# Kernel optimization log

Hardware: AMD Instinct MI355X
Metric: run time of the kernel (lower is better)

## Reference

```python
import jax, jax.numpy as jnp
import numpy as np

N = 100000   # num nodes
E = 20000    # num hyperedges
D = 128      # feature dim
NNZ = 600000 # incidences
EPS = 1e-5


def setup_inputs() -> dict:
    key = jax.random.key(0)
    ks = jax.random.split(key, 16)
    src = jax.random.randint(ks[0], (NNZ,), 0, N)   # node indices
    edg = jax.random.randint(ks[1], (NNZ,), 0, E)   # hyperedge indices
    edge_index = jnp.stack([src, edg]).astype(jnp.int64)
    node_attr = jax.random.normal(ks[2], (N, D), jnp.float32)
    edge_attr = jax.random.normal(ks[3], (E, D), jnp.float32)  # unused by forward
    inp = {"edge_index": edge_index, "node_attr": node_attr, "edge_attr": edge_attr}
    for l in range(3):
        inp[f"W{l+1}"] = jax.random.normal(ks[4 + l], (D, D), jnp.float32) / np.float32(np.sqrt(D))
        inp[f"b{l+1}"] = jnp.zeros((D,), jnp.float32)
        inp[f"g{l+1}"] = jnp.ones((D,), jnp.float32)
        inp[f"beta{l+1}"] = jnp.zeros((D,), jnp.float32)
    return inp


def _hconv(x, W, b, src, edg):
    # PyG HypergraphConv (no attention): out = D^{-1} H W_e B^{-1} H^T (X Theta) + b, W_e = I
    x = x @ W
    ones = jnp.ones(src.shape, x.dtype)
    deg_n = jax.ops.segment_sum(ones, src, num_segments=N)  # node degree
    deg_e = jax.ops.segment_sum(ones, edg, num_segments=E)  # hyperedge size
    Dinv = jnp.where(deg_n > 0, 1.0 / deg_n, 0.0)
    Binv = jnp.where(deg_e > 0, 1.0 / deg_e, 0.0)
    # node -> hyperedge: m_e = B^{-1} sum_{i in e} x_i
    e_feat = Binv[:, None] * jax.ops.segment_sum(x[src], edg, num_segments=E)
    # hyperedge -> node: out_i = D^{-1} sum_{e ni i} m_e
    out = Dinv[:, None] * jax.ops.segment_sum(e_feat[edg], src, num_segments=N)
    return out + b


def _bn(x, g, beta):
    # BatchNorm1d, training mode (biased variance over nodes)
    mu = jnp.mean(x, axis=0)
    var = jnp.mean((x - mu) ** 2, axis=0)
    return g * (x - mu) / jnp.sqrt(var + EPS) + beta


def reference(edge_index, node_attr, edge_attr,
              W1, b1, g1, beta1, W2, b2, g2, beta2, W3, b3, g3, beta3):
    src, edg = edge_index[0], edge_index[1]
    x = _bn(jax.nn.relu(_hconv(node_attr, W1, b1, src, edg)), g1, beta1)
    x = _bn(jax.nn.relu(_hconv(x, W2, b2, src, edg)), g2, beta2)
    x = _bn(jax.nn.relu(_hconv(x, W3, b3, src, edg)), g3, beta3)
    return x
```

## Files before the change

### kernel.cpp

```cpp
#include <hip/hip_runtime.h>
#include <stdint.h>

#define DIM 128

static inline int cdiv(long a, long b) { return (int)((a + b - 1) / b); }

typedef float f32x4 __attribute__((ext_vector_type(4)));

__device__ __forceinline__ unsigned pk_bf16(float a, float b) {
  unsigned ua = __float_as_uint(a), ub = __float_as_uint(b);
  ua = (ua + 0x7FFFu + ((ua >> 16) & 1u)) >> 16;
  ub = (ub + 0x7FFFu + ((ub >> 16) & 1u)) >> 16;
  return ua | (ub << 16);
}
__device__ __forceinline__ float bf_lo(unsigned u) { return __uint_as_float(u << 16); }
__device__ __forceinline__ float bf_hi(unsigned u) { return __uint_as_float(u & 0xFFFF0000u); }

__global__ __launch_bounds__(256) void convert_idx_kernel(
    const int* __restrict__ raw, int* __restrict__ out, long n_total) {
  bool is64;
  {
    int l = threadIdx.x & 63;
    int v = raw[2 * l + 1];
    unsigned long long m = __ballot(v == 0);
    is64 = (m == ~0ull);
  }
  long i = blockIdx.x * 256L + threadIdx.x;
  if (i < n_total) out[i] = is64 ? raw[2 * i] : raw[i];
}

__global__ __launch_bounds__(256) void count_kernel(
    const int* __restrict__ src, const int* __restrict__ edg,
    int* __restrict__ cnt, int E, int nnz) {
  int g = blockIdx.x * 256 + threadIdx.x;
  if (g < nnz) {
    atomicAdd(&cnt[edg[g]], 1);
    atomicAdd(&cnt[E + src[g]], 1);
  }
}

__global__ __launch_bounds__(256) void scanA_kernel(
    const int* __restrict__ cnt, int* __restrict__ P, int* __restrict__ BS, int M) {
  __shared__ int lds[256];
  int t = threadIdx.x;
  long base = blockIdx.x * 1024L;
  int v[4], ts = 0;
#pragma unroll
  for (int j = 0; j < 4; ++j) {
    long i = base + t * 4 + j;
    v[j] = (i < M) ? cnt[i] : 0;
    ts += v[j];
  }
  lds[t] = ts;
  __syncthreads();
  for (int off = 1; off < 256; off <<= 1) {
    int x = (t >= off) ? lds[t - off] : 0;
    __syncthreads();
    lds[t] += x;
    __syncthreads();
  }
  int run = lds[t] - ts;
#pragma unroll
  for (int j = 0; j < 4; ++j) {
    long i = base + t * 4 + j;
    if (i < M) P[i] = run;
    run += v[j];
  }
  if (t == 255) BS[blockIdx.x] = lds[255];
}

__global__ void scanB_kernel(int* __restrict__ BS, int* __restrict__ P,
                             int nblocks, int M) {
  if (threadIdx.x == 0) {
    int run = 0;
    for (int i = 0; i < nblocks; ++i) { int x = BS[i]; BS[i] = run; run += x; }
    P[M] = run;
  }
}

__global__ __launch_bounds__(256) void scanC_kernel(
    int* __restrict__ P, const int* __restrict__ BS, int M) {
  long i = blockIdx.x * 256L + threadIdx.x;
  if (i < M) P[i] += BS[i >> 10];
}

__global__ __launch_bounds__(256) void fill_adj_kernel(
    const int* __restrict__ src, const int* __restrict__ edg,
    const int* __restrict__ P, int* __restrict__ cnt,
    int* __restrict__ adj_e, int* __restrict__ adj_n, int E, int nnz) {
  int g = blockIdx.x * 256 + threadIdx.x;
  if (g < nnz) {
    int e = edg[g], s = src[g];
    int pe = P[e] + atomicAdd(&cnt[e], 1);
    adj_e[pe] = s;
    int pn = P[E + s] - nnz + atomicAdd(&cnt[E + s], 1);
    adj_n[pn] = e;
  }
}

__global__ void prep_w_kernel(const float* __restrict__ W,
                              const float* __restrict__ aff_a,
                              const float* __restrict__ aff_d,
                              float* __restrict__ Wp, float* __restrict__ rvec,
                              int has_aff) {
  int j = threadIdx.x;
  float racc = 0.0f;
  for (int c = 0; c < DIM; ++c) {
    float w = W[c * DIM + j];
    float a = has_aff ? aff_a[c] : 1.0f;
    float d = has_aff ? aff_d[c] : 0.0f;
    Wp[c * DIM + j] = a * w;
    racc = fmaf(d, w, racc);
  }
  rvec[j] = racc;
}

__global__ __launch_bounds__(256) void cast_x_kernel(
    const float* __restrict__ X, uint2* __restrict__ xh, long total4) {
  long i = blockIdx.x * 256L + threadIdx.x;
  if (i >= total4) return;
  float4 v = ((const float4*)X)[i];
  uint2 o;
  o.x = pk_bf16(v.x, v.y);
  o.y = pk_bf16(v.z, v.w);
  xh[i] = o;
}

__global__ __launch_bounds__(256) void edge_gather_kernel(
    const uint2* __restrict__ xh, const int* __restrict__ P,
    const int* __restrict__ adj_e, float* __restrict__ ag, int E, int SENT) {
  int slot = threadIdx.x >> 5;
  int l = threadIdx.x & 31;
  int e = blockIdx.x * 8 + slot;
  if (e >= E) return;
  int p0 = P[e], p1 = P[e + 1];
  float4 a = {0.f, 0.f, 0.f, 0.f};
  int kl = p1 - 1;
  for (int k = p0; k < p1; k += 8) {
    int n0 = adj_e[min(k, kl)];
    int n1 = (k + 1 <= kl) ? adj_e[k + 1] : SENT;
    int n2 = (k + 2 <= kl) ? adj_e[k + 2] : SENT;
    int n3 = (k + 3 <= kl) ? adj_e[k + 3] : SENT;
    int n4 = (k + 4 <= kl) ? adj_e[k + 4] : SENT;
    int n5 = (k + 5 <= kl) ? adj_e[k + 5] : SENT;
    int n6 = (k + 6 <= kl) ? adj_e[k + 6] : SENT;
    int n7 = (k + 7 <= kl) ? adj_e[k + 7] : SENT;
    uint2 q0 = xh[(size_t)n0 * 32 + l];
    uint2 q1 = xh[(size_t)n1 * 32 + l];
    uint2 q2 = xh[(size_t)n2 * 32 + l];
    uint2 q3 = xh[(size_t)n3 * 32 + l];
    uint2 q4 = xh[(size_t)n4 * 32 + l];
    uint2 q5 = xh[(size_t)n5 * 32 + l];
    uint2 q6 = xh[(size_t)n6 * 32 + l];
    uint2 q7 = xh[(size_t)n7 * 32 + l];
    a.x += ((bf_lo(q0.x) + bf_lo(q1.x)) + (bf_lo(q2.x) + bf_lo(q3.x))) +
           ((bf_lo(q4.x) + bf_lo(q5.x)) + (bf_lo(q6.x) + bf_lo(q7.x)));
    a.y += ((bf_hi(q0.x) + bf_hi(q1.x)) + (bf_hi(q2.x) + bf_hi(q3.x))) +
           ((bf_hi(q4.x) + bf_hi(q5.x)) + (bf_hi(q6.x) + bf_hi(q7.x)));
    a.z += ((bf_lo(q0.y) + bf_lo(q1.y)) + (bf_lo(q2.y) + bf_lo(q3.y))) +
           ((bf_lo(q4.y) + bf_lo(q5.y)) + (bf_lo(q6.y) + bf_lo(q7.y)));
    a.w += ((bf_hi(q0.y) + bf_hi(q1.y)) + (bf_hi(q2.y) + bf_hi(q3.y))) +
           ((bf_hi(q4.y) + bf_hi(q5.y)) + (bf_hi(q6.y) + bf_hi(q7.y)));
  }
  float binv = (p1 > p0) ? 1.0f / (float)(p1 - p0) : 0.0f;
  float4 o;
  o.x = a.x * binv; o.y = a.y * binv; o.z = a.z * binv; o.w = a.w * binv;
  ((float4*)ag)[(size_t)e * 32 + l] = o;
}

__global__ __launch_bounds__(256) void gemm128_kernel(
    const float* __restrict__ X, const float* __restrict__ Wp,
    const float* __restrict__ rvec, const int* __restrict__ Pdeg,
    unsigned* __restrict__ Yh, int nrows) {
  __shared__ float sW[32 * DIM];
  __shared__ float sX[DIM * 36];
  const int t = threadIdx.x;
  const int row0 = blockIdx.x * DIM;
  const int tx = t & 15, ty = t >> 4;
  const int col0 = tx * 8, lr0 = ty * 8;
  float acc[8][8];
#pragma unroll
  for (int i = 0; i < 8; ++i)
#pragma unroll
    for (int j = 0; j < 8; ++j) acc[i][j] = 0.0f;

  for (int kc = 0; kc < 4; ++kc) {
    __syncthreads();
    {
      const float4* W4 = (const float4*)(Wp + kc * 32 * DIM);
      float4* sW4 = (float4*)sW;
#pragma unroll
      for (int i = 0; i < 4; ++i) sW4[t + i * 256] = W4[t + i * 256];
    }
#pragma unroll
    for (int i = 0; i < 4; ++i) {
      int q = t + i * 256;
      int rr = q >> 3, kq = q & 7;
      int gr = row0 + rr; if (gr >= nrows) gr = nrows - 1;
      float4 v = *(const float4*)&X[(size_t)gr * DIM + kc * 32 + kq * 4];
      *(float4*)&sX[rr * 36 + kq * 4] = v;
    }
    __syncthreads();
    for (int kk = 0; kk < 32; ++kk) {
      float4 w0 = *(const float4*)&sW[kk * DIM + col0];
      float4 w1 = *(const float4*)&sW[kk * DIM + col0 + 4];
      float wv[8] = {w0.x, w0.y, w0.z, w0.w, w1.x, w1.y, w1.z, w1.w};
      float xv[8];
#pragma unroll
      for (int i = 0; i < 8; ++i) xv[i] = sX[(lr0 + i) * 36 + kk];
#pragma unroll
      for (int i = 0; i < 8; ++i)
#pragma unroll
        for (int j = 0; j < 8; ++j) acc[i][j] = fmaf(xv[i], wv[j], acc[i][j]);
    }
  }
  float4 r0 = *(const float4*)&rvec[col0];
  float4 r1 = *(const float4*)&rvec[col0 + 4];
#pragma unroll
  for (int i = 0; i < 8; ++i) {
    int gr = row0 + lr0 + i;
    if (gr < nrows) {
      float nz = (Pdeg[gr + 1] > Pdeg[gr]) ? 1.0f : 0.0f;
      float o0x = (acc[i][0] + r0.x) * nz, o0y = (acc[i][1] + r0.y) * nz;
      float o0z = (acc[i][2] + r0.z) * nz, o0w = (acc[i][3] + r0.w) * nz;
      float o1x = (acc[i][4] + r1.x) * nz, o1y = (acc[i][5] + r1.y) * nz;
      float o1z = (acc[i][6] + r1.z) * nz, o1w = (acc[i][7] + r1.w) * nz;
      uint4 st;
      st.x = pk_bf16(o0x, o0y);
      st.y = pk_bf16(o0z, o0w);
      st.z = pk_bf16(o1x, o1y);
      st.w = pk_bf16(o1z, o1w);
      *(uint4*)&Yh[(size_t)gr * 64 + (col0 >> 1)] = st;
    }
  }
}

__global__ __launch_bounds__(256) void node_gather_kernel(
    const uint2* __restrict__ ef, const int* __restrict__ P,
    const int* __restrict__ adj_n, const float* __restrict__ b,
    uint2* __restrict__ zh, float* __restrict__ sum,
    float* __restrict__ sumsq, int E, int N, int nnz, int SENT) {
  __shared__ float lsum[DIM], lsumsq[DIM];
  int t = threadIdx.x;
  if (t < DIM) { lsum[t] = 0.f; lsumsq[t] = 0.f; }
  __syncthreads();
  int slot = t >> 5;
  int l = t & 31;
  float4 bc = ((const float4*)b)[l];
  float4 s1 = {0.f, 0.f, 0.f, 0.f}, s2 = {0.f, 0.f, 0.f, 0.f};
  for (int i = blockIdx.x * 8 + slot; i < N; i += gridDim.x * 8) {
    int p0 = P[E + i] - nnz, p1 = P[E + i + 1] - nnz;
    float4 a = {0.f, 0.f, 0.f, 0.f};
    int kl = p1 - 1;
    for (int k = p0; k < p1; k += 8) {
      int e0 = adj_n[min(k, kl)];
      int e1 = (k + 1 <= kl) ? adj_n[k + 1] : SENT;
      int e2 = (k + 2 <= kl) ? adj_n[k + 2] : SENT;
      int e3 = (k + 3 <= kl) ? adj_n[k + 3] : SENT;
      int e4 = (k + 4 <= kl) ? adj_n[k + 4] : SENT;
      int e5 = (k + 5 <= kl) ? adj_n[k + 5] : SENT;
      int e6 = (k + 6 <= kl) ? adj_n[k + 6] : SENT;
      int e7 = (k + 7 <= kl) ? adj_n[k + 7] : SENT;
      uint2 q0 = ef[(size_t)e0 * 32 + l];
      uint2 q1 = ef[(size_t)e1 * 32 + l];
      uint2 q2 = ef[(size_t)e2 * 32 + l];
      uint2 q3 = ef[(size_t)e3 * 32 + l];
      uint2 q4 = ef[(size_t)e4 * 32 + l];
      uint2 q5 = ef[(size_t)e5 * 32 + l];
      uint2 q6 = ef[(size_t)e6 * 32 + l];
      uint2 q7 = ef[(size_t)e7 * 32 + l];
      a.x += ((bf_lo(q0.x) + bf_lo(q1.x)) + (bf_lo(q2.x) + bf_lo(q3.x))) +
             ((bf_lo(q4.x) + bf_lo(q5.x)) + (bf_lo(q6.x) + bf_lo(q7.x)));
      a.y += ((bf_hi(q0.x) + bf_hi(q1.x)) + (bf_hi(q2.x) + bf_hi(q3.x))) +
             ((bf_hi(q4.x) + bf_hi(q5.x)) + (bf_hi(q6.x) + bf_hi(q7.x)));
      a.z += ((bf_lo(q0.y) + bf_lo(q1.y)) + (bf_lo(q2.y) + bf_lo(q3.y))) +
             ((bf_lo(q4.y) + bf_lo(q5.y)) + (bf_lo(q6.y) + bf_lo(q7.y)));
      a.w += ((bf_hi(q0.y) + bf_hi(q1.y)) + (bf_hi(q2.y) + bf_hi(q3.y))) +
             ((bf_hi(q4.y) + bf_hi(q5.y)) + (bf_hi(q6.y) + bf_hi(q7.y)));
    }
    float dinv = (p1 > p0) ? 1.0f / (float)(p1 - p0) : 0.0f;
    float4 v;
    v.x = fmaxf(fmaf(dinv, a.x, bc.x), 0.f);
    v.y = fmaxf(fmaf(dinv, a.y, bc.y), 0.f);
    v.z = fmaxf(fmaf(dinv, a.z, bc.z), 0.f);
    v.w = fmaxf(fmaf(dinv, a.w, bc.w), 0.f);
    uint2 o;
    o.x = pk_bf16(v.x, v.y);
    o.y = pk_bf16(v.z, v.w);
    zh[(size_t)i * 32 + l] = o;
    s1.x += v.x; s1.y += v.y; s1.z += v.z; s1.w += v.w;
    s2.x = fmaf(v.x, v.x, s2.x); s2.y = fmaf(v.y, v.y, s2.y);
    s2.z = fmaf(v.z, v.z, s2.z); s2.w = fmaf(v.w, v.w, s2.w);
  }
  int c0 = l * 4;
  atomicAdd(&lsum[c0 + 0], s1.x); atomicAdd(&lsum[c0 + 1], s1.y);
  atomicAdd(&lsum[c0 + 2], s1.z); atomicAdd(&lsum[c0 + 3], s1.w);
  atomicAdd(&lsumsq[c0 + 0], s2.x); atomicAdd(&lsumsq[c0 + 1], s2.y);
  atomicAdd(&lsumsq[c0 + 2], s2.z); atomicAdd(&lsumsq[c0 + 3], s2.w);
  __syncthreads();
  if (t < DIM) {
    atomicAdd(&sum[t], lsum[t]);
    atomicAdd(&sumsq[t], lsumsq[t]);
  }
}

__global__ void finalize_bn_kernel(const float* __restrict__ sum,
                                   const float* __restrict__ sumsq,
                                   const float* __restrict__ g,
                                   const float* __restrict__ beta,
                                   float* __restrict__ aff_a, float* __restrict__ aff_d,
                                   int n) {
  int c = threadIdx.x;
  float inv_n = 1.0f / (float)n;
  float mu = sum[c] * inv_n;
  float var = fmaf(sumsq[c], inv_n, -mu * mu);
  float a = g[c] * rsqrtf(var + 1e-5f);
  aff_a[c] = a;
  aff_d[c] = fmaf(-mu, a, beta[c]);
}

__global__ __launch_bounds__(256) void apply_affine_kernel(
    const uint2* __restrict__ zh, const float* __restrict__ aff_a,
    const float* __restrict__ aff_d, float* __restrict__ out, long total4) {
  long i = blockIdx.x * 256L + threadIdx.x;
  if (i >= total4) return;
  int c4 = (int)(i & 31);
  float4 a = ((const float4*)aff_a)[c4];
  float4 d = ((const float4*)aff_d)[c4];
  uint2 q = zh[i];
  f32x4 o;
  o.x = fmaf(a.x, bf_lo(q.x), d.x);
  o.y = fmaf(a.y, bf_hi(q.x), d.y);
  o.z = fmaf(a.z, bf_lo(q.y), d.z);
  o.w = fmaf(a.w, bf_hi(q.y), d.w);
  __builtin_nontemporal_store(o, &((f32x4*)out)[i]);
}

extern "C" void kernel_launch(void* const* d_in, const int* in_sizes, int n_in,
                              void* d_out, int out_size, void* d_ws, size_t ws_size,
                              hipStream_t stream) {
  const int NNZv = in_sizes[0] / 2;
  const int Nv   = in_sizes[1] / DIM;
  const int Ev   = in_sizes[2] / DIM;
  const int* eidx_raw = (const int*)d_in[0];
  const float* node_attr = (const float*)d_in[1];

  float* bufE  = (float*)d_ws;
  float* Wp    = bufE + (size_t)Ev * DIM;
  float* rvec  = Wp + DIM * DIM;
  float* sums  = rvec + 128;
  float* sumsq = sums + 128;
  float* aff_a = sumsq + 128;
  float* aff_d = aff_a + 128;
  int* src   = (int*)(aff_d + 128);
  int* edg   = src + NNZv;
  int* cnt   = edg + NNZv;
  int* P     = cnt + (((size_t)Ev + Nv + 3) & ~(size_t)3);
  int* BS    = P + (((size_t)Ev + Nv + 1 + 3) & ~(size_t)3);
  int* adj_e = BS + 256;
  int* adj_n = adj_e + NNZv;
  unsigned* efh = (unsigned*)src;
  uint2* xh = (uint2*)(adj_n + NNZv);

  const int M = Ev + Nv;
  const int nbA = cdiv(M, 1024);

  convert_idx_kernel<<<cdiv(2L * NNZv, 256), 256, 0, stream>>>(eidx_raw, src, 2L * NNZv);
  hipMemsetAsync(cnt, 0, (size_t)M * 4, stream);
  count_kernel<<<cdiv(NNZv, 256), 256, 0, stream>>>(src, edg, cnt, Ev, NNZv);
  scanA_kernel<<<nbA, 256, 0, stream>>>(cnt, P, BS, M);
  scanB_kernel<<<1, 64, 0, stream>>>(BS, P, nbA, M);
  scanC_kernel<<<cdiv(M, 256), 256, 0, stream>>>(P, BS, M);
  hipMemsetAsync(cnt, 0, (size_t)M * 4, stream);
  fill_adj_kernel<<<cdiv(NNZv, 256), 256, 0, stream>>>(src, edg, P, cnt, adj_e, adj_n, Ev, NNZv);
  cast_x_kernel<<<cdiv((long)Nv * 32, 256), 256, 0, stream>>>(node_attr, xh, (long)Nv * 32);
  hipMemsetAsync(efh + (size_t)Ev * 64, 0, 256, stream);
  hipMemsetAsync(xh + (size_t)Nv * 32, 0, 256, stream);

  for (int l = 0; l < 3; ++l) {
    const float* W    = (const float*)d_in[3 + l * 4];
    const float* b    = (const float*)d_in[4 + l * 4];
    const float* g    = (const float*)d_in[5 + l * 4];
    const float* beta = (const float*)d_in[6 + l * 4];

    prep_w_kernel<<<1, 128, 0, stream>>>(W, aff_a, aff_d, Wp, rvec, l > 0 ? 1 : 0);
    edge_gather_kernel<<<cdiv(Ev, 8), 256, 0, stream>>>(xh, P, adj_e, bufE, Ev, Nv);
    gemm128_kernel<<<cdiv(Ev, DIM), 256, 0, stream>>>(bufE, Wp, rvec, P, efh, Ev);
    hipMemsetAsync(sums, 0, 256 * 4, stream);
    node_gather_kernel<<<2048, 256, 0, stream>>>(
        (const uint2*)efh, P, adj_n, b, xh, sums, sumsq, Ev, Nv, NNZv, Ev);
    finalize_bn_kernel<<<1, 128, 0, stream>>>(sums, sumsq, g, beta, aff_a, aff_d, Nv);
  }
  apply_affine_kernel<<<cdiv((long)Nv * 32, 256), 256, 0, stream>>>(
      xh, aff_a, aff_d, (float*)d_out, (long)Nv * 32);
}
```

Measured before the change: 827.7 us.

## Fuse index conversion, BN finalize and input cast into neighbouring kernels

Folds index dtype conversion into the counting kernel and computes the BatchNorm affine inside the weight-prep kernel, so the per-layer finalize launch is dropped. Layer 0 gathers directly from the fp32 input, which removes the separate bf16 cast pass and its extra write. Padded gather slots now repeat the last neighbour and subtract its contribution afterwards instead of reading a zeroed sentinel row, which removes the sentinel memsets. Node gather switches from a grid-stride loop to one-row-per-slot launching. Edge features are written with nontemporal stores. The changes reduce launches and memory passes but add a tail correction load per row and can introduce small cancellation error.

```diff
diff --git a/kernel.cpp b/kernel.cpp
--- a/kernel.cpp
+++ b/kernel.cpp
@@ -16,8 +16,9 @@
 __device__ __forceinline__ float bf_lo(unsigned u) { return __uint_as_float(u << 16); }
 __device__ __forceinline__ float bf_hi(unsigned u) { return __uint_as_float(u & 0xFFFF0000u); }
 
-__global__ __launch_bounds__(256) void convert_idx_kernel(
-    const int* __restrict__ raw, int* __restrict__ out, long n_total) {
+__global__ __launch_bounds__(256) void count_kernel(
+    const int* __restrict__ raw, int* __restrict__ src, int* __restrict__ edg,
+    int* __restrict__ cnt, int E, int nnz) {
   bool is64;
   {
     int l = threadIdx.x & 63;
@@ -25,17 +26,14 @@
     unsigned long long m = __ballot(v == 0);
     is64 = (m == ~0ull);
   }
-  long i = blockIdx.x * 256L + threadIdx.x;
-  if (i < n_total) out[i] = is64 ? raw[2 * i] : raw[i];
-}
-
-__global__ __launch_bounds__(256) void count_kernel(
-    const int* __restrict__ src, const int* __restrict__ edg,
-    int* __restrict__ cnt, int E, int nnz) {
   int g = blockIdx.x * 256 + threadIdx.x;
   if (g < nnz) {
-    atomicAdd(&cnt[edg[g]], 1);
-    atomicAdd(&cnt[E + src[g]], 1);
+    int s = is64 ? raw[2 * g] : raw[g];
+    int e = is64 ? raw[2 * (nnz + g)] : raw[nnz + g];
+    src[g] = s;
+    edg[g] = e;
+    atomicAdd(&cnt[e], 1);
+    atomicAdd(&cnt[E + s], 1);
   }
 }
 
@@ -99,36 +97,37 @@
 }
 
 __global__ void prep_w_kernel(const float* __restrict__ W,
-                              const float* __restrict__ aff_a,
-                              const float* __restrict__ aff_d,
+                              const float* __restrict__ sums,
+                              const float* __restrict__ sumsq,
+                              const float* __restrict__ gprev,
+                              const float* __restrict__ betaprev,
                               float* __restrict__ Wp, float* __restrict__ rvec,
-                              int has_aff) {
+                              int has_aff, float inv_n) {
+  __shared__ float sa[DIM], sd[DIM];
   int j = threadIdx.x;
+  if (has_aff) {
+    float mu = sums[j] * inv_n;
+    float var = fmaf(sumsq[j], inv_n, -mu * mu);
+    float a = gprev[j] * rsqrtf(var + 1e-5f);
+    sa[j] = a;
+    sd[j] = fmaf(-mu, a, betaprev[j]);
+  } else {
+    sa[j] = 1.0f;
+    sd[j] = 0.0f;
+  }
+  __syncthreads();
   float racc = 0.0f;
   for (int c = 0; c < DIM; ++c) {
     float w = W[c * DIM + j];
-    float a = has_aff ? aff_a[c] : 1.0f;
-    float d = has_aff ? aff_d[c] : 0.0f;
-    Wp[c * DIM + j] = a * w;
-    racc = fmaf(d, w, racc);
+    Wp[c * DIM + j] = sa[c] * w;
+    racc = fmaf(sd[c], w, racc);
   }
   rvec[j] = racc;
 }
 
-__global__ __launch_bounds__(256) void cast_x_kernel(
-    const float* __restrict__ X, uint2* __restrict__ xh, long total4) {
-  long i = blockIdx.x * 256L + threadIdx.x;
-  if (i >= total4) return;
-  float4 v = ((const float4*)X)[i];
-  uint2 o;
-  o.x = pk_bf16(v.x, v.y);
-  o.y = pk_bf16(v.z, v.w);
-  xh[i] = o;
-}
-
-__global__ __launch_bounds__(256) void edge_gather_kernel(
-    const uint2* __restrict__ xh, const int* __restrict__ P,
-    const int* __restrict__ adj_e, float* __restrict__ ag, int E, int SENT) {
+__global__ __launch_bounds__(256) void edge_gather_f32_kernel(
+    const float4* __restrict__ X4, const int* __restrict__ P,
+    const int* __restrict__ adj_e, float* __restrict__ ag, int E) {
   int slot = threadIdx.x >> 5;
   int l = threadIdx.x & 31;
   int e = blockIdx.x * 8 + slot;
@@ -138,13 +137,60 @@
   int kl = p1 - 1;
   for (int k = p0; k < p1; k += 8) {
     int n0 = adj_e[min(k, kl)];
-    int n1 = (k + 1 <= kl) ? adj_e[k + 1] : SENT;
-    int n2 = (k + 2 <= kl) ? adj_e[k + 2] : SENT;
-    int n3 = (k + 3 <= kl) ? adj_e[k + 3] : SENT;
-    int n4 = (k + 4 <= kl) ? adj_e[k + 4] : SENT;
-    int n5 = (k + 5 <= kl) ? adj_e[k + 5] : SENT;
-    int n6 = (k + 6 <= kl) ? adj_e[k + 6] : SENT;
-    int n7 = (k + 7 <= kl) ? adj_e[k + 7] : SENT;
+    int n1 = adj_e[min(k + 1, kl)];
+    int n2 = adj_e[min(k + 2, kl)];
+    int n3 = adj_e[min(k + 3, kl)];
+    int n4 = adj_e[min(k + 4, kl)];
+    int n5 = adj_e[min(k + 5, kl)];
+    int n6 = adj_e[min(k + 6, kl)];
+    int n7 = adj_e[min(k + 7, kl)];
+    float4 q0 = X4[(size_t)n0 * 32 + l];
+    float4 q1 = X4[(size_t)n1 * 32 + l];
+    float4 q2 = X4[(size_t)n2 * 32 + l];
+    float4 q3 = X4[(size_t)n3 * 32 + l];
+    float4 q4 = X4[(size_t)n4 * 32 + l];
+    float4 q5 = X4[(size_t)n5 * 32 + l];
+    float4 q6 = X4[(size_t)n6 * 32 + l];
+    float4 q7 = X4[(size_t)n7 * 32 + l];
+    a.x += ((q0.x + q1.x) + (q2.x + q3.x)) + ((q4.x + q5.x) + (q6.x + q7.x));
+    a.y += ((q0.y + q1.y) + (q2.y + q3.y)) + ((q4.y + q5.y) + (q6.y + q7.y));
+    a.z += ((q0.z + q1.z) + (q2.z + q3.z)) + ((q4.z + q5.z) + (q6.z + q7.z));
+    a.w += ((q0.w + q1.w) + (q2.w + q3.w)) + ((q4.w + q5.w) + (q6.w + q7.w));
+  }
+  int deg = p1 - p0;
+  if (deg > 0) {
+    int extra = ((deg + 7) & ~7) - deg;
+    if (extra) {
+      float4 ql = X4[(size_t)adj_e[kl] * 32 + l];
+      float ex = (float)extra;
+      a.x -= ex * ql.x; a.y -= ex * ql.y; a.z -= ex * ql.z; a.w -= ex * ql.w;
+    }
+  }
+  float binv = (deg > 0) ? 1.0f / (float)deg : 0.0f;
+  f32x4 o;
+  o.x = a.x * binv; o.y = a.y * binv; o.z = a.z * binv; o.w = a.w * binv;
+  __builtin_nontemporal_store(o, &((f32x4*)ag)[(size_t)e * 32 + l]);
+}
+
+__global__ __launch_bounds__(256) void edge_gather_bf16_kernel(
+    const uint2* __restrict__ xh, const int* __restrict__ P,
+    const int* __restrict__ adj_e, float* __restrict__ ag, int E) {
+  int slot = threadIdx.x >> 5;
+  int l = threadIdx.x & 31;
+  int e = blockIdx.x * 8 + slot;
+  if (e >= E) return;
+  int p0 = P[e], p1 = P[e + 1];
+  float4 a = {0.f, 0.f, 0.f, 0.f};
+  int kl = p1 - 1;
+  for (int k = p0; k < p1; k += 8) {
+    int n0 = adj_e[min(k, kl)];
+    int n1 = adj_e[min(k + 1, kl)];
+    int n2 = adj_e[min(k + 2, kl)];
+    int n3 = adj_e[min(k + 3, kl)];
+    int n4 = adj_e[min(k + 4, kl)];
+    int n5 = adj_e[min(k + 5, kl)];
+    int n6 = adj_e[min(k + 6, kl)];
+    int n7 = adj_e[min(k + 7, kl)];
     uint2 q0 = xh[(size_t)n0 * 32 + l];
     uint2 q1 = xh[(size_t)n1 * 32 + l];
     uint2 q2 = xh[(size_t)n2 * 32 + l];
@@ -162,10 +208,20 @@
     a.w += ((bf_hi(q0.y) + bf_hi(q1.y)) + (bf_hi(q2.y) + bf_hi(q3.y))) +
            ((bf_hi(q4.y) + bf_hi(q5.y)) + (bf_hi(q6.y) + bf_hi(q7.y)));
   }
-  float binv = (p1 > p0) ? 1.0f / (float)(p1 - p0) : 0.0f;
-  float4 o;
+  int deg = p1 - p0;
+  if (deg > 0) {
+    int extra = ((deg + 7) & ~7) - deg;
+    if (extra) {
+      uint2 ql = xh[(size_t)adj_e[kl] * 32 + l];
+      float ex = (float)extra;
+      a.x -= ex * bf_lo(ql.x); a.y -= ex * bf_hi(ql.x);
+      a.z -= ex * bf_lo(ql.y); a.w -= ex * bf_hi(ql.y);
+    }
+  }
+  float binv = (deg > 0) ? 1.0f / (float)deg : 0.0f;
+  f32x4 o;
   o.x = a.x * binv; o.y = a.y * binv; o.z = a.z * binv; o.w = a.w * binv;
-  ((float4*)ag)[(size_t)e * 32 + l] = o;
+  __builtin_nontemporal_store(o, &((f32x4*)ag)[(size_t)e * 32 + l]);
 }
 
 __global__ __launch_bounds__(256) void gemm128_kernel(
@@ -239,28 +295,29 @@
     const uint2* __restrict__ ef, const int* __restrict__ P,
     const int* __restrict__ adj_n, const float* __restrict__ b,
     uint2* __restrict__ zh, float* __restrict__ sum,
-    float* __restrict__ sumsq, int E, int N, int nnz, int SENT) {
+    float* __restrict__ sumsq, int E, int N, int nnz) {
   __shared__ float lsum[DIM], lsumsq[DIM];
   int t = threadIdx.x;
   if (t < DIM) { lsum[t] = 0.f; lsumsq[t] = 0.f; }
   __syncthreads();
   int slot = t >> 5;
   int l = t & 31;
-  float4 bc = ((const float4*)b)[l];
   float4 s1 = {0.f, 0.f, 0.f, 0.f}, s2 = {0.f, 0.f, 0.f, 0.f};
-  for (int i = blockIdx.x * 8 + slot; i < N; i += gridDim.x * 8) {
+  int i = blockIdx.x * 8 + slot;
+  if (i < N) {
+    float4 bc = ((const float4*)b)[l];
     int p0 = P[E + i] - nnz, p1 = P[E + i + 1] - nnz;
     float4 a = {0.f, 0.f, 0.f, 0.f};
     int kl = p1 - 1;
     for (int k = p0; k < p1; k += 8) {
       int e0 = adj_n[min(k, kl)];
-      int e1 = (k + 1 <= kl) ? adj_n[k + 1] : SENT;
-      int e2 = (k + 2 <= kl) ? adj_n[k + 2] : SENT;
-      int e3 = (k + 3 <= kl) ? adj_n[k + 3] : SENT;
-      int e4 = (k + 4 <= kl) ? adj_n[k + 4] : SENT;
-      int e5 = (k + 5 <= kl) ? adj_n[k + 5] : SENT;
-      int e6 = (k + 6 <= kl) ? adj_n[k + 6] : SENT;
-      int e7 = (k + 7 <= kl) ? adj_n[k + 7] : SENT;
+      int e1 = adj_n[min(k + 1, kl)];
+      int e2 = adj_n[min(k + 2, kl)];
+      int e3 = adj_n[min(k + 3, kl)];
+      int e4 = adj_n[min(k + 4, kl)];
+      int e5 = adj_n[min(k + 5, kl)];
+      int e6 = adj_n[min(k + 6, kl)];
+      int e7 = adj_n[min(k + 7, kl)];
       uint2 q0 = ef[(size_t)e0 * 32 + l];
       uint2 q1 = ef[(size_t)e1 * 32 + l];
       uint2 q2 = ef[(size_t)e2 * 32 + l];
@@ -278,7 +335,17 @@
       a.w += ((bf_hi(q0.y) + bf_hi(q1.y)) + (bf_hi(q2.y) + bf_hi(q3.y))) +
              ((bf_hi(q4.y) + bf_hi(q5.y)) + (bf_hi(q6.y) + bf_hi(q7.y)));
     }
-    float dinv = (p1 > p0) ? 1.0f / (float)(p1 - p0) : 0.0f;
+    int deg = p1 - p0;
+    if (deg > 0) {
+      int extra = ((deg + 7) & ~7) - deg;
+      if (extra) {
+        uint2 ql = ef[(size_t)adj_n[kl] * 32 + l];
+        float ex = (float)extra;
+        a.x -= ex * bf_lo(ql.x); a.y -= ex * bf_hi(ql.x);
+        a.z -= ex * bf_lo(ql.y); a.w -= ex * bf_hi(ql.y);
+      }
+    }
+    float dinv = (deg > 0) ? 1.0f / (float)deg : 0.0f;
     float4 v;
     v.x = fmaxf(fmaf(dinv, a.x, bc.x), 0.f);
     v.y = fmaxf(fmaf(dinv, a.y, bc.y), 0.f);
@@ -364,32 +431,39 @@
 
   const int M = Ev + Nv;
   const int nbA = cdiv(M, 1024);
-
-  convert_idx_kernel<<<cdiv(2L * NNZv, 256), 256, 0, stream>>>(eidx_raw, src, 2L * NNZv);
+  const float inv_n = 1.0f / (float)Nv;
+
   hipMemsetAsync(cnt, 0, (size_t)M * 4, stream);
-  count_kernel<<<cdiv(NNZv, 256), 256, 0, stream>>>(src, edg, cnt, Ev, NNZv);
+  count_kernel<<<cdiv(NNZv, 256), 256, 0, stream>>>(eidx_raw, src, edg, cnt, Ev, NNZv);
   scanA_kernel<<<nbA, 256, 0, stream>>>(cnt, P, BS, M);
   scanB_kernel<<<1, 64, 0, stream>>>(BS, P, nbA, M);
   scanC_kernel<<<cdiv(M, 256), 256, 0, stream>>>(P, BS, M);
   hipMemsetAsync(cnt, 0, (size_t)M * 4, stream);
   fill_adj_kernel<<<cdiv(NNZv, 256), 256, 0, stream>>>(src, edg, P, cnt, adj_e, adj_n, Ev, NNZv);
-  cast_x_kernel<<<cdiv((long)Nv * 32, 256), 256, 0, stream>>>(node_attr, xh, (long)Nv * 32);
-  hipMemsetAsync(efh + (size_t)Ev * 64, 0, 256, stream);
-  hipMemsetAsync(xh + (size_t)Nv * 32, 0, 256, stream);
 
   for (int l = 0; l < 3; ++l) {
-    const float* W    = (const float*)d_in[3 + l * 4];
-    const float* b    = (const float*)d_in[4 + l * 4];
-    const float* g    = (const float*)d_in[5 + l * 4];
-    const float* beta = (const float*)d_in[6 + l * 4];
-
-    prep_w_kernel<<<1, 128, 0, stream>>>(W, aff_a, aff_d, Wp, rvec, l > 0 ? 1 : 0);
-    edge_gather_kernel<<<cdiv(Ev, 8), 256, 0, stream>>>(xh, P, adj_e, bufE, Ev, Nv);
+    const float* W     = (const float*)d_in[3 + l * 4];
+    const float* b     = (const float*)d_in[4 + l * 4];
+    const float* gprev    = (const float*)d_in[5 + (l > 0 ? l - 1 : 0) * 4];
+    const float* betaprev = (const float*)d_in[6 + (l > 0 ? l - 1 : 0) * 4];
+
+    prep_w_kernel<<<1, 128, 0, stream>>>(W, sums, sumsq, gprev, betaprev,
+                                         Wp, rvec, l > 0 ? 1 : 0, inv_n);
+    if (l == 0)
+      edge_gather_f32_kernel<<<cdiv(Ev, 8), 256, 0, stream>>>(
+          (const float4*)node_attr, P, adj_e, bufE, Ev);
+    else
+      edge_gather_bf16_kernel<<<cdiv(Ev, 8), 256, 0, stream>>>(
+          xh, P, adj_e, bufE, Ev);
     gemm128_kernel<<<cdiv(Ev, DIM), 256, 0, stream>>>(bufE, Wp, rvec, P, efh, Ev);
     hipMemsetAsync(sums, 0, 256 * 4, stream);
-    node_gather_kernel<<<2048, 256, 0, stream>>>(
-        (const uint2*)efh, P, adj_n, b, xh, sums, sumsq, Ev, Nv, NNZv, Ev);
-    finalize_bn_kernel<<<1, 128, 0, stream>>>(sums, sumsq, g, beta, aff_a, aff_d, Nv);
+    node_gather_kernel<<<cdiv(Nv, 8), 256, 0, stream>>>(
+        (const uint2*)efh, P, adj_n, b, xh, sums, sumsq, Ev, Nv, NNZv);
+  }
+  {
+    const float* g2    = (const float*)d_in[5 + 2 * 4];
+    const float* beta2 = (const float*)d_in[6 + 2 * 4];
+    finalize_bn_kernel<<<1, 128, 0, stream>>>(sums, sumsq, g2, beta2, aff_a, aff_d, Nv);
   }
   apply_affine_kernel<<<cdiv((long)Nv * 32, 256), 256, 0, stream>>>(
       xh, aff_a, aff_d, (float*)d_out, (long)Nv * 32);
```

New measurement: 1.484 ms. +79.2%, slower.
